# Optimization experiments

Hardware: AMD Instinct MI355X
Metric: run time of the kernel (lower is better)

## Reference

```python
import jax, jax.numpy as jnp
import numpy as np

N_HEAD = 16

def setup_inputs() -> dict:
    key = jax.random.key(0)
    ks = jax.random.split(key, 5)
    B, S, C = 4, 2048, 1024
    x = jax.random.normal(ks[0], (B, S, C), dtype=jnp.float32)
    w_qkv = jax.random.normal(ks[1], (C, 3 * C), dtype=jnp.float32) * (1.0 / np.sqrt(C))
    b_qkv = jnp.zeros((3 * C,), dtype=jnp.float32)
    w_proj = jax.random.normal(ks[2], (C, C), dtype=jnp.float32) * (1.0 / np.sqrt(C))
    b_proj = jnp.zeros((C,), dtype=jnp.float32)
    return {"x": x, "w_qkv": w_qkv, "b_qkv": b_qkv, "w_proj": w_proj, "b_proj": b_proj}

def reference(x, w_qkv, b_qkv, w_proj, b_proj):
    B, S, C = x.shape
    H = N_HEAD
    D = C // H
    qkv = x @ w_qkv + b_qkv                       # [B,S,3C]
    q, k, v = jnp.split(qkv, 3, axis=-1)
    # [B,S,C] -> [B,H,S,D]
    q = q.reshape(B, S, H, D).transpose(0, 2, 1, 3)
    k = k.reshape(B, S, H, D).transpose(0, 2, 1, 3)
    v = v.reshape(B, S, H, D).transpose(0, 2, 1, 3)
    scores = jnp.einsum('bhqd,bhkd->bhqk', q, k) / jnp.sqrt(jnp.float32(D))
    causal = jnp.tril(jnp.ones((S, S), dtype=bool))
    scores = jnp.where(causal[None, None], scores, -jnp.inf)
    weights = jax.nn.softmax(scores, axis=-1)     # dropout p=0 -> identity
    out = jnp.einsum('bhqk,bhkd->bhqd', weights, v)
    out = out.transpose(0, 2, 1, 3).reshape(B, S, C)
    return out @ w_proj + b_proj
```

## Files before the change

### kernel.cpp

```cpp
#include <hip/hip_runtime.h>

#define SDIM 2048
#define CDIM 1024
#define BDIM 4
#define HDIM 16
#define DDIM 64

#define ATT_SCALE 0.18033688011112042f

typedef __attribute__((ext_vector_type(8))) short bf16x8;
typedef __attribute__((ext_vector_type(4))) short bf16x4;
typedef __attribute__((ext_vector_type(4))) float f32x4;
typedef unsigned short u16;

#define MFMA __builtin_amdgcn_mfma_f32_16x16x32_bf16
#define LDS_ORDER_FENCE() __asm__ __volatile__("" ::: "memory")

__device__ __forceinline__ u16 f2b(float f) {
    union { float f; unsigned u; } v; v.f = f;
    unsigned r = v.u + 0x7FFFu + ((v.u >> 16) & 1u);
    return (u16)(r >> 16);
}
__device__ __forceinline__ u16 f2b_trunc(float f) {
    union { float f; unsigned u; } v; v.f = f;
    return (u16)(v.u >> 16);
}

typedef const __attribute__((address_space(1))) unsigned int* gas_t;
typedef __attribute__((address_space(3))) unsigned int* las_t;
__device__ __forceinline__ void cp16(const void* g, void* l) {
    __builtin_amdgcn_global_load_lds((gas_t)g, (las_t)l, 16, 0, 0);
}

__device__ __forceinline__ float fast_exp2(float x) {
#if __has_builtin(__builtin_amdgcn_exp2f)
    return __builtin_amdgcn_exp2f(x);
#else
    return __exp2f(x);
#endif
}

__global__ __launch_bounds__(256) void conv_cast(
    const float* __restrict__ src, u16* __restrict__ dst)
{
    int i = (blockIdx.x * 256 + threadIdx.x) * 8;
    float4 a = *reinterpret_cast<const float4*>(&src[i]);
    float4 b = *reinterpret_cast<const float4*>(&src[i + 4]);
    u16 u[8];
    u[0]=f2b(a.x); u[1]=f2b(a.y); u[2]=f2b(a.z); u[3]=f2b(a.w);
    u[4]=f2b(b.x); u[5]=f2b(b.y); u[6]=f2b(b.z); u[7]=f2b(b.w);
    *reinterpret_cast<uint4*>(&dst[i]) = *reinterpret_cast<uint4*>(u);
}

__global__ __launch_bounds__(256) void conv_t(
    const float* __restrict__ src, u16* __restrict__ dst, int K, int N)
{
    __shared__ __align__(16) u16 t[64][72];
    const int tid = threadIdx.x;
    const int k0 = blockIdx.y * 64, n0 = blockIdx.x * 64;
#pragma unroll
    for (int it = 0; it < 4; it++) {
        int c = tid + it * 256;
        int r = c >> 4, c4 = (c & 15) * 4;
        float4 f = *reinterpret_cast<const float4*>(&src[(size_t)(k0 + r) * N + n0 + c4]);
        t[c4 + 0][r] = f2b(f.x);
        t[c4 + 1][r] = f2b(f.y);
        t[c4 + 2][r] = f2b(f.z);
        t[c4 + 3][r] = f2b(f.w);
    }
    __syncthreads();
#pragma unroll
    for (int it = 0; it < 2; it++) {
        int c = tid + it * 256;
        int r = c >> 3, c8 = (c & 7) * 8;
        *reinterpret_cast<uint4*>(&dst[(size_t)(n0 + r) * K + k0 + c8]) =
            *reinterpret_cast<const uint4*>(&t[r][c8]);
    }
}

__global__ __launch_bounds__(256, 4) void gemm_qkv(
    const u16* __restrict__ A, const u16* __restrict__ Bt,
    const float* __restrict__ bias,
    u16* __restrict__ Qb, u16* __restrict__ Kb, u16* __restrict__ Vtb)
{
    __shared__ __align__(16) u16 As[128 * 32];
    __shared__ __align__(16) u16 Bs[128 * 32];
    __shared__ __align__(16) u16 Eb[4][16 * 68];
    const int tid = threadIdx.x, lane = tid & 63, wave = tid >> 6;
    const int wm = wave >> 1, wn = wave & 1;
    const int l16 = lane & 15, quad = lane >> 4;
    const int m0 = blockIdx.y * 128, n0 = blockIdx.x * 128;
    const int K = CDIM;

    const int cl0 = wave * 128 + lane;
    const int r0 = cl0 >> 2, c0 = cl0 & 3;
    const int r1 = r0 + 16;

    f32x4 acc[4][4];
#pragma unroll
    for (int i = 0; i < 4; i++)
#pragma unroll
        for (int j = 0; j < 4; j++) acc[i][j] = (f32x4){0.f, 0.f, 0.f, 0.f};

    for (int k0 = 0; k0 < K; k0 += 32) {
        __syncthreads();
        cp16(&A [(size_t)(m0 + r0) * K + k0 + c0 * 8], &As[wave * 1024]);
        cp16(&A [(size_t)(m0 + r1) * K + k0 + c0 * 8], &As[wave * 1024 + 512]);
        cp16(&Bt[(size_t)(n0 + r0) * K + k0 + c0 * 8], &Bs[wave * 1024]);
        cp16(&Bt[(size_t)(n0 + r1) * K + k0 + c0 * 8], &Bs[wave * 1024 + 512]);
        __syncthreads();

        bf16x8 a[4], b[4];
#pragma unroll
        for (int i = 0; i < 4; i++)
            a[i] = *reinterpret_cast<const bf16x8*>(&As[((wm * 64 + i * 16 + l16) * 4 + quad) * 8]);
#pragma unroll
        for (int j = 0; j < 4; j++)
            b[j] = *reinterpret_cast<const bf16x8*>(&Bs[((wn * 64 + j * 16 + l16) * 4 + quad) * 8]);
#pragma unroll
        for (int i = 0; i < 4; i++)
#pragma unroll
            for (int j = 0; j < 4; j++)
                acc[i][j] = MFMA(a[i], b[j], acc[i][j], 0, 0, 0);
    }

    const int mm0 = m0 + wm * 64;
    const int bidx = mm0 >> 11, s0 = mm0 & 2047;
    const int n_base = n0 + wn * 64;
    u16* eb = &Eb[wave][0];
    const int erow = lane >> 2, ec = (lane & 3) * 16;

    if (n0 >= 2 * CDIM) {
        const int h = (n_base - 2 * CDIM) >> 6;
        const size_t gb = ((size_t)(bidx * HDIM + h)) * DDIM * SDIM;
#pragma unroll
        for (int j = 0; j < 4; j++) {
            float bvj = bias[n_base + j * 16 + l16];
            LDS_ORDER_FENCE();
#pragma unroll
            for (int i = 0; i < 4; i++)
#pragma unroll
                for (int r = 0; r < 4; r++)
                    eb[l16 * 68 + i * 16 + quad * 4 + r] = f2b(acc[i][j][r] + bvj);
            LDS_ORDER_FENCE();
            union { bf16x4 hp[4]; uint4 u[2]; } pk;
            pk.hp[0] = *reinterpret_cast<const bf16x4*>(&eb[erow * 68 + ec]);
            pk.hp[1] = *reinterpret_cast<const bf16x4*>(&eb[erow * 68 + ec + 4]);
            pk.hp[2] = *reinterpret_cast<const bf16x4*>(&eb[erow * 68 + ec + 8]);
            pk.hp[3] = *reinterpret_cast<const bf16x4*>(&eb[erow * 68 + ec + 12]);
            u16* gp = &Vtb[gb + (size_t)(j * 16 + erow) * SDIM + s0 + ec];
            *reinterpret_cast<uint4*>(gp)     = pk.u[0];
            *reinterpret_cast<uint4*>(gp + 8) = pk.u[1];
        }
    } else {
        const bool isK = (n_base >= CDIM);
        u16* dst = isK ? Kb : Qb;
        const float scale = isK ? 1.0f : ATT_SCALE;
        const int hh = (n_base & 1023) >> 6;
        const size_t hb = ((size_t)(bidx * HDIM + hh)) * SDIM;
        float bvj[4];
#pragma unroll
        for (int j = 0; j < 4; j++) bvj[j] = bias[n_base + j * 16 + l16];
#pragma unroll
        for (int i = 0; i < 4; i++) {
            LDS_ORDER_FENCE();
#pragma unroll
            for (int j = 0; j < 4; j++)
#pragma unroll
                for (int r = 0; r < 4; r++)
                    eb[(quad * 4 + r) * 68 + j * 16 + l16] =
                        f2b((acc[i][j][r] + bvj[j]) * scale);
            LDS_ORDER_FENCE();
            union { bf16x4 hp[4]; uint4 u[2]; } pk;
            pk.hp[0] = *reinterpret_cast<const bf16x4*>(&eb[erow * 68 + ec]);
            pk.hp[1] = *reinterpret_cast<const bf16x4*>(&eb[erow * 68 + ec + 4]);
            pk.hp[2] = *reinterpret_cast<const bf16x4*>(&eb[erow * 68 + ec + 8]);
            pk.hp[3] = *reinterpret_cast<const bf16x4*>(&eb[erow * 68 + ec + 12]);
            const int s = s0 + i * 16 + erow;
            u16* gp = &dst[(hb + s) * DDIM + ec];
            *reinterpret_cast<uint4*>(gp)     = pk.u[0];
            *reinterpret_cast<uint4*>(gp + 8) = pk.u[1];
        }
    }
}

__global__ __launch_bounds__(512, 6) void attn(
    const u16* __restrict__ Qb, const u16* __restrict__ Kb,
    const u16* __restrict__ Vtb, u16* __restrict__ Ob)
{
    __shared__ __align__(16) u16 Ks[2][64 * 64];
    __shared__ __align__(16) u16 Vts[2][64 * 64];
    __shared__ __align__(16) u16 Ps[8][16 * 68];

    const int tid = threadIdx.x;
    const int lane = tid & 63, wave = tid >> 6;
    const int l16 = lane & 15, quad = lane >> 4;
    const int x = blockIdx.x;
    const int bh = (x & 7) * 8 + ((x >> 3) & 7);
    const int qt = 15 - (x >> 6);
    const int q0 = qt * 128;
    const int b = bh >> 4, h = bh & 15;
    const size_t base = (size_t)bh * (SDIM * DDIM);

    const int cl0 = wave * 64 + lane;
    const int sr0 = cl0 >> 3, scc = cl0 & 7;
    const int sg0 = scc ^ (sr0 & 7);

    const int qrow = q0 + wave * 16 + l16;
    bf16x8 aq0 = *reinterpret_cast<const bf16x8*>(&Qb[base + (size_t)qrow * DDIM + quad * 8]);
    bf16x8 aq1 = *reinterpret_cast<const bf16x8*>(&Qb[base + (size_t)qrow * DDIM + 32 + quad * 8]);

    u16* Pw = &Ps[wave][0];

    f32x4 O[4];
    f32x4 Osum = (f32x4){0.f, 0.f, 0.f, 0.f};
#pragma unroll
    for (int j = 0; j < 4; j++) O[j] = (f32x4){0.f, 0.f, 0.f, 0.f};
    const short onev = (l16 == 0) ? (short)0x3F80 : (short)0;
    const bf16x8 bones = {onev, onev, onev, onev, onev, onev, onev, onev};

    const int nkb = (qt + 1) * 2;
    const int Arow = q0 + wave * 16;

    cp16(&Kb [base + (size_t)sr0 * DDIM + sg0 * 8], &Ks[0][wave * 512]);
    cp16(&Vtb[base + (size_t)sr0 * SDIM + sg0 * 8], &Vts[0][wave * 512]);

    for (int kbi = 0; kbi < nkb; kbi++) {
        const int cur = kbi & 1;
        const int kb = kbi * 64;
        __syncthreads();
        if (kbi + 1 < nkb) {
            const int kb2 = kb + 64;
            cp16(&Kb [base + (size_t)(kb2 + sr0) * DDIM + sg0 * 8], &Ks[1 - cur][wave * 512]);
            cp16(&Vtb[base + (size_t)sr0 * SDIM + kb2 + sg0 * 8], &Vts[1 - cur][wave * 512]);
        }
        if (kb > Arow + 15) continue;

        const u16* Kc = &Ks[cur][0];
        const u16* Vc = &Vts[cur][0];

        f32x4 sc[4];
#pragma unroll
        for (int j = 0; j < 4; j++) {
            int kr = j * 16 + l16;
            bf16x8 bk0 = *reinterpret_cast<const bf16x8*>(&Kc[(kr * 8 + ( quad      ^ (kr & 7))) * 8]);
            bf16x8 bk1 = *reinterpret_cast<const bf16x8*>(&Kc[(kr * 8 + ((quad + 4) ^ (kr & 7))) * 8]);
            f32x4 s = (f32x4){0.f, 0.f, 0.f, 0.f};
            s = MFMA(aq0, bk0, s, 0, 0, 0);
            s = MFMA(aq1, bk1, s, 0, 0, 0);
            sc[j] = s;
        }
        if (kb + 63 > Arow) {
            const int qrel = Arow - kb;
#pragma unroll
            for (int j = 0; j < 4; j++) {
                int kk = j * 16 + l16;
#pragma unroll
                for (int r = 0; r < 4; r++)
                    sc[j][r] = (kk <= qrel + quad * 4 + r) ? sc[j][r] : -1e30f;
            }
        }
#pragma unroll
        for (int j = 0; j < 4; j++)
#pragma unroll
            for (int r = 0; r < 4; r++) {
                float p = fast_exp2(sc[j][r]);
                Pw[(quad * 4 + r) * 68 + j * 16 + l16] = f2b_trunc(p);
            }
        LDS_ORDER_FENCE();
        union { bf16x4 hp[2]; bf16x8 f; } a0u, a1u;
        a0u.hp[0] = *reinterpret_cast<const bf16x4*>(&Pw[l16 * 68 + quad * 8]);
        a0u.hp[1] = *reinterpret_cast<const bf16x4*>(&Pw[l16 * 68 + quad * 8 + 4]);
        a1u.hp[0] = *reinterpret_cast<const bf16x4*>(&Pw[l16 * 68 + 32 + quad * 8]);
        a1u.hp[1] = *reinterpret_cast<const bf16x4*>(&Pw[l16 * 68 + 32 + quad * 8 + 4]);

#pragma unroll
        for (int j = 0; j < 4; j++) {
            int vr = j * 16 + l16;
            bf16x8 bv0 = *reinterpret_cast<const bf16x8*>(&Vc[(vr * 8 + ( quad      ^ (vr & 7))) * 8]);
            bf16x8 bv1 = *reinterpret_cast<const bf16x8*>(&Vc[(vr * 8 + ((quad + 4) ^ (vr & 7))) * 8]);
            O[j] = MFMA(a0u.f, bv0, O[j], 0, 0, 0);
            O[j] = MFMA(a1u.f, bv1, O[j], 0, 0, 0);
        }
        Osum = MFMA(a0u.f, bones, Osum, 0, 0, 0);
        Osum = MFMA(a1u.f, bones, Osum, 0, 0, 0);
    }

#pragma unroll
    for (int r = 0; r < 4; r++) {
        float l = __shfl(Osum[r], (lane & 48));
        float inv = 1.0f / l;
        int s = q0 + wave * 16 + quad * 4 + r;
#pragma unroll
        for (int j = 0; j < 4; j++)
            Ob[((size_t)(b * SDIM + s)) * CDIM + h * 64 + j * 16 + l16] =
                f2b(O[j][r] * inv);
    }
}

__global__ __launch_bounds__(256) void gemm_proj(
    const u16* __restrict__ A, const u16* __restrict__ Bt,
    const float* __restrict__ bias, float* __restrict__ out)
{
    __shared__ __align__(16) u16 As[128 * 32];
    __shared__ __align__(16) u16 Bs[128 * 32];
    const int tid = threadIdx.x, lane = tid & 63, wave = tid >> 6;
    const int wm = wave >> 1, wn = wave & 1;
    const int l16 = lane & 15, quad = lane >> 4;
    const int m0 = blockIdx.y * 128, n0 = blockIdx.x * 128;
    const int K = CDIM, N = CDIM;

    const int cl0 = wave * 128 + lane;
    const int r0 = cl0 >> 2, c0 = cl0 & 3;
    const int r1 = r0 + 16;

    f32x4 acc[4][4];
#pragma unroll
    for (int i = 0; i < 4; i++)
#pragma unroll
        for (int j = 0; j < 4; j++) acc[i][j] = (f32x4){0.f, 0.f, 0.f, 0.f};

    for (int k0 = 0; k0 < K; k0 += 32) {
        __syncthreads();
        cp16(&A [(size_t)(m0 + r0) * K + k0 + c0 * 8], &As[wave * 1024]);
        cp16(&A [(size_t)(m0 + r1) * K + k0 + c0 * 8], &As[wave * 1024 + 512]);
        cp16(&Bt[(size_t)(n0 + r0) * K + k0 + c0 * 8], &Bs[wave * 1024]);
        cp16(&Bt[(size_t)(n0 + r1) * K + k0 + c0 * 8], &Bs[wave * 1024 + 512]);
        __syncthreads();

        bf16x8 a[4], b[4];
#pragma unroll
        for (int i = 0; i < 4; i++)
            a[i] = *reinterpret_cast<const bf16x8*>(&As[((wm * 64 + i * 16 + l16) * 4 + quad) * 8]);
#pragma unroll
        for (int j = 0; j < 4; j++)
            b[j] = *reinterpret_cast<const bf16x8*>(&Bs[((wn * 64 + j * 16 + l16) * 4 + quad) * 8]);
#pragma unroll
        for (int i = 0; i < 4; i++)
#pragma unroll
            for (int j = 0; j < 4; j++)
                acc[i][j] = MFMA(a[i], b[j], acc[i][j], 0, 0, 0);
    }

#pragma unroll
    for (int i = 0; i < 4; i++) {
        int mbase = m0 + wm * 64 + i * 16 + quad * 4;
#pragma unroll
        for (int j = 0; j < 4; j++) {
            int n = n0 + wn * 64 + j * 16 + l16;
            float bv = bias[n];
#pragma unroll
            for (int r = 0; r < 4; r++)
                out[(size_t)(mbase + r) * N + n] = acc[i][j][r] + bv;
        }
    }
}

extern "C" void kernel_launch(void* const* d_in, const int* in_sizes, int n_in,
                              void* d_out, int out_size, void* d_ws, size_t ws_size,
                              hipStream_t stream) {
    const float* x      = (const float*)d_in[0];
    const float* w_qkv  = (const float*)d_in[1];
    const float* b_qkv  = (const float*)d_in[2];
    const float* w_proj = (const float*)d_in[3];
    const float* b_proj = (const float*)d_in[4];
    float* out = (float*)d_out;

    const size_t per = (size_t)BDIM * HDIM * SDIM * DDIM;
    u16* Qb  = (u16*)d_ws;
    u16* Kb  = Qb + per;
    u16* Vtb = Kb + per;
    u16* Ob  = Vtb + per;
    u16* Xb  = Ob;
    u16* WqT = Ob + per;
    u16* WpT = WqT + (size_t)3 * CDIM * CDIM;

    dim3 blk(256);
    conv_cast<<<dim3(per / (256 * 8)), blk, 0, stream>>>(x, Xb);
    conv_t<<<dim3(3 * CDIM / 64, CDIM / 64), blk, 0, stream>>>(w_qkv, WqT, CDIM, 3 * CDIM);
    conv_t<<<dim3(CDIM / 64, CDIM / 64), blk, 0, stream>>>(w_proj, WpT, CDIM, CDIM);

    gemm_qkv<<<dim3(3 * CDIM / 128, BDIM * SDIM / 128), blk, 0, stream>>>(
        Xb, WqT, b_qkv, Qb, Kb, Vtb);
    attn<<<dim3(BDIM * HDIM * (SDIM / 128)), dim3(512), 0, stream>>>(Qb, Kb, Vtb, Ob);
    gemm_proj<<<dim3(CDIM / 128, BDIM * SDIM / 128), blk, 0, stream>>>(
        Ob, WpT, b_proj, out);
}
```

Measured before the change: 253.7 us.

## Double GEMM K-tile to 64 with XOR-swizzled LDS and merge prep kernels

Both bf16 GEMMs (QKV and output projection) now stage 64-wide K tiles instead of 32. This halves the number of barrier pairs per K loop. The LDS layout uses an XOR swizzle on the 16-byte chunk index so the MFMA fragment reads avoid bank conflicts. The three conversion/transpose kernels are merged into one launch to cut launch overhead, and gemm_proj gets an occupancy hint; the larger LDS footprint may lower occupancy.

```diff
diff --git a/kernel.cpp b/kernel.cpp
--- a/kernel.cpp
+++ b/kernel.cpp
@@ -40,24 +40,37 @@
 #endif
 }
 
-__global__ __launch_bounds__(256) void conv_cast(
-    const float* __restrict__ src, u16* __restrict__ dst)
-{
-    int i = (blockIdx.x * 256 + threadIdx.x) * 8;
-    float4 a = *reinterpret_cast<const float4*>(&src[i]);
-    float4 b = *reinterpret_cast<const float4*>(&src[i + 4]);
-    u16 u[8];
-    u[0]=f2b(a.x); u[1]=f2b(a.y); u[2]=f2b(a.z); u[3]=f2b(a.w);
-    u[4]=f2b(b.x); u[5]=f2b(b.y); u[6]=f2b(b.z); u[7]=f2b(b.w);
-    *reinterpret_cast<uint4*>(&dst[i]) = *reinterpret_cast<uint4*>(u);
-}
-
-__global__ __launch_bounds__(256) void conv_t(
-    const float* __restrict__ src, u16* __restrict__ dst, int K, int N)
+__global__ __launch_bounds__(256) void prep(
+    const float* __restrict__ x, const float* __restrict__ w_qkv,
+    const float* __restrict__ w_proj,
+    u16* __restrict__ Xb, u16* __restrict__ WqT, u16* __restrict__ WpT)
 {
     __shared__ __align__(16) u16 t[64][72];
+    const int bx = blockIdx.x;
     const int tid = threadIdx.x;
-    const int k0 = blockIdx.y * 64, n0 = blockIdx.x * 64;
+
+    if (bx < 4096) {
+        int i = (bx * 256 + tid) * 8;
+        float4 a = *reinterpret_cast<const float4*>(&x[i]);
+        float4 b = *reinterpret_cast<const float4*>(&x[i + 4]);
+        u16 u[8];
+        u[0]=f2b(a.x); u[1]=f2b(a.y); u[2]=f2b(a.z); u[3]=f2b(a.w);
+        u[4]=f2b(b.x); u[5]=f2b(b.y); u[6]=f2b(b.z); u[7]=f2b(b.w);
+        *reinterpret_cast<uint4*>(&Xb[i]) = *reinterpret_cast<uint4*>(u);
+        return;
+    }
+
+    const float* src; u16* dst; int N, n0, k0;
+    if (bx < 4096 + 768) {
+        int b2 = bx - 4096;
+        src = w_qkv; dst = WqT; N = 3 * CDIM;
+        n0 = (b2 % 48) * 64; k0 = (b2 / 48) * 64;
+    } else {
+        int b2 = bx - 4864;
+        src = w_proj; dst = WpT; N = CDIM;
+        n0 = (b2 % 16) * 64; k0 = (b2 / 16) * 64;
+    }
+    const int K = CDIM;
 #pragma unroll
     for (int it = 0; it < 4; it++) {
         int c = tid + it * 256;
@@ -83,8 +96,8 @@
     const float* __restrict__ bias,
     u16* __restrict__ Qb, u16* __restrict__ Kb, u16* __restrict__ Vtb)
 {
-    __shared__ __align__(16) u16 As[128 * 32];
-    __shared__ __align__(16) u16 Bs[128 * 32];
+    __shared__ __align__(16) u16 As[128 * 64];
+    __shared__ __align__(16) u16 Bs[128 * 64];
     __shared__ __align__(16) u16 Eb[4][16 * 68];
     const int tid = threadIdx.x, lane = tid & 63, wave = tid >> 6;
     const int wm = wave >> 1, wn = wave & 1;
@@ -92,9 +105,8 @@
     const int m0 = blockIdx.y * 128, n0 = blockIdx.x * 128;
     const int K = CDIM;
 
-    const int cl0 = wave * 128 + lane;
-    const int r0 = cl0 >> 2, c0 = cl0 & 3;
-    const int r1 = r0 + 16;
+    const int l8 = lane & 7, lr = lane >> 3;
+    const int sg = l8 ^ lr;
 
     f32x4 acc[4][4];
 #pragma unroll
@@ -102,26 +114,37 @@
 #pragma unroll
         for (int j = 0; j < 4; j++) acc[i][j] = (f32x4){0.f, 0.f, 0.f, 0.f};
 
-    for (int k0 = 0; k0 < K; k0 += 32) {
+    for (int k0 = 0; k0 < K; k0 += 64) {
         __syncthreads();
-        cp16(&A [(size_t)(m0 + r0) * K + k0 + c0 * 8], &As[wave * 1024]);
-        cp16(&A [(size_t)(m0 + r1) * K + k0 + c0 * 8], &As[wave * 1024 + 512]);
-        cp16(&Bt[(size_t)(n0 + r0) * K + k0 + c0 * 8], &Bs[wave * 1024]);
-        cp16(&Bt[(size_t)(n0 + r1) * K + k0 + c0 * 8], &Bs[wave * 1024 + 512]);
+#pragma unroll
+        for (int u = 0; u < 4; u++) {
+            int row = wave * 32 + u * 8 + lr;
+            cp16(&A [(size_t)(m0 + row) * K + k0 + sg * 8], &As[(wave * 4 + u) * 512]);
+            cp16(&Bt[(size_t)(n0 + row) * K + k0 + sg * 8], &Bs[(wave * 4 + u) * 512]);
+        }
         __syncthreads();
 
-        bf16x8 a[4], b[4];
-#pragma unroll
-        for (int i = 0; i < 4; i++)
-            a[i] = *reinterpret_cast<const bf16x8*>(&As[((wm * 64 + i * 16 + l16) * 4 + quad) * 8]);
-#pragma unroll
-        for (int j = 0; j < 4; j++)
-            b[j] = *reinterpret_cast<const bf16x8*>(&Bs[((wn * 64 + j * 16 + l16) * 4 + quad) * 8]);
-#pragma unroll
-        for (int i = 0; i < 4; i++)
-#pragma unroll
-            for (int j = 0; j < 4; j++)
-                acc[i][j] = MFMA(a[i], b[j], acc[i][j], 0, 0, 0);
+#pragma unroll
+        for (int kk = 0; kk < 2; kk++) {
+            bf16x8 a[4], b[4];
+#pragma unroll
+            for (int i = 0; i < 4; i++) {
+                int row = wm * 64 + i * 16 + l16;
+                a[i] = *reinterpret_cast<const bf16x8*>(
+                    &As[(row * 8 + ((kk * 4 + quad) ^ (l16 & 7))) * 8]);
+            }
+#pragma unroll
+            for (int j = 0; j < 4; j++) {
+                int row = wn * 64 + j * 16 + l16;
+                b[j] = *reinterpret_cast<const bf16x8*>(
+                    &Bs[(row * 8 + ((kk * 4 + quad) ^ (l16 & 7))) * 8]);
+            }
+#pragma unroll
+            for (int i = 0; i < 4; i++)
+#pragma unroll
+                for (int j = 0; j < 4; j++)
+                    acc[i][j] = MFMA(a[i], b[j], acc[i][j], 0, 0, 0);
+        }
     }
 
     const int mm0 = m0 + wm * 64;
@@ -298,21 +321,20 @@
     }
 }
 
-__global__ __launch_bounds__(256) void gemm_proj(
+__global__ __launch_bounds__(256, 4) void gemm_proj(
     const u16* __restrict__ A, const u16* __restrict__ Bt,
     const float* __restrict__ bias, float* __restrict__ out)
 {
-    __shared__ __align__(16) u16 As[128 * 32];
-    __shared__ __align__(16) u16 Bs[128 * 32];
+    __shared__ __align__(16) u16 As[128 * 64];
+    __shared__ __align__(16) u16 Bs[128 * 64];
     const int tid = threadIdx.x, lane = tid & 63, wave = tid >> 6;
     const int wm = wave >> 1, wn = wave & 1;
     const int l16 = lane & 15, quad = lane >> 4;
     const int m0 = blockIdx.y * 128, n0 = blockIdx.x * 128;
     const int K = CDIM, N = CDIM;
 
-    const int cl0 = wave * 128 + lane;
-    const int r0 = cl0 >> 2, c0 = cl0 & 3;
-    const int r1 = r0 + 16;
+    const int l8 = lane & 7, lr = lane >> 3;
+    const int sg = l8 ^ lr;
 
     f32x4 acc[4][4];
 #pragma unroll
@@ -320,26 +342,37 @@
 #pragma unroll
         for (int j = 0; j < 4; j++) acc[i][j] = (f32x4){0.f, 0.f, 0.f, 0.f};
 
-    for (int k0 = 0; k0 < K; k0 += 32) {
+    for (int k0 = 0; k0 < K; k0 += 64) {
         __syncthreads();
-        cp16(&A [(size_t)(m0 + r0) * K + k0 + c0 * 8], &As[wave * 1024]);
-        cp16(&A [(size_t)(m0 + r1) * K + k0 + c0 * 8], &As[wave * 1024 + 512]);
-        cp16(&Bt[(size_t)(n0 + r0) * K + k0 + c0 * 8], &Bs[wave * 1024]);
-        cp16(&Bt[(size_t)(n0 + r1) * K + k0 + c0 * 8], &Bs[wave * 1024 + 512]);
+#pragma unroll
+        for (int u = 0; u < 4; u++) {
+            int row = wave * 32 + u * 8 + lr;
+            cp16(&A [(size_t)(m0 + row) * K + k0 + sg * 8], &As[(wave * 4 + u) * 512]);
+            cp16(&Bt[(size_t)(n0 + row) * K + k0 + sg * 8], &Bs[(wave * 4 + u) * 512]);
+        }
         __syncthreads();
 
-        bf16x8 a[4], b[4];
-#pragma unroll
-        for (int i = 0; i < 4; i++)
-            a[i] = *reinterpret_cast<const bf16x8*>(&As[((wm * 64 + i * 16 + l16) * 4 + quad) * 8]);
-#pragma unroll
-        for (int j = 0; j < 4; j++)
-            b[j] = *reinterpret_cast<const bf16x8*>(&Bs[((wn * 64 + j * 16 + l16) * 4 + quad) * 8]);
-#pragma unroll
-        for (int i = 0; i < 4; i++)
-#pragma unroll
-            for (int j = 0; j < 4; j++)
-                acc[i][j] = MFMA(a[i], b[j], acc[i][j], 0, 0, 0);
+#pragma unroll
+        for (int kk = 0; kk < 2; kk++) {
+            bf16x8 a[4], b[4];
+#pragma unroll
+            for (int i = 0; i < 4; i++) {
+                int row = wm * 64 + i * 16 + l16;
+                a[i] = *reinterpret_cast<const bf16x8*>(
+                    &As[(row * 8 + ((kk * 4 + quad) ^ (l16 & 7))) * 8]);
+            }
+#pragma unroll
+            for (int j = 0; j < 4; j++) {
+                int row = wn * 64 + j * 16 + l16;
+                b[j] = *reinterpret_cast<const bf16x8*>(
+                    &Bs[(row * 8 + ((kk * 4 + quad) ^ (l16 & 7))) * 8]);
+            }
+#pragma unroll
+            for (int i = 0; i < 4; i++)
+#pragma unroll
+                for (int j = 0; j < 4; j++)
+                    acc[i][j] = MFMA(a[i], b[j], acc[i][j], 0, 0, 0);
+        }
     }
 
 #pragma unroll
@@ -376,9 +409,7 @@
     u16* WpT = WqT + (size_t)3 * CDIM * CDIM;
 
     dim3 blk(256);
-    conv_cast<<<dim3(per / (256 * 8)), blk, 0, stream>>>(x, Xb);
-    conv_t<<<dim3(3 * CDIM / 64, CDIM / 64), blk, 0, stream>>>(w_qkv, WqT, CDIM, 3 * CDIM);
-    conv_t<<<dim3(CDIM / 64, CDIM / 64), blk, 0, stream>>>(w_proj, WpT, CDIM, CDIM);
+    prep<<<dim3(4096 + 768 + 256), blk, 0, stream>>>(x, w_qkv, w_proj, Xb, WqT, WpT);
 
     gemm_qkv<<<dim3(3 * CDIM / 128, BDIM * SDIM / 128), blk, 0, stream>>>(
         Xb, WqT, b_qkv, Qb, Kb, Vtb);
```

Result: faster. 246.7 us (-2.8%).
